# Optimization experiments

Measured on AMD Instinct MI355X. Metric: run time of the kernel, lower is better.

The kernel has to match this reference:

```python
import jax, jax.numpy as jnp
import numpy as np
import math

WINDOW = 2048
EMBED = 1024
BATCH = 8


def setup_inputs() -> dict:
    key = jax.random.key(0)
    ks = jax.random.split(key, 7)
    s = 1.0 / math.sqrt(EMBED)
    return {
        "embeddings": jax.random.normal(ks[0], (BATCH, WINDOW, EMBED), dtype=jnp.float32),
        "Wq": jax.random.uniform(ks[1], (EMBED, EMBED), jnp.float32, -s, s),
        "bq": jax.random.uniform(ks[2], (EMBED,), jnp.float32, -s, s),
        "Wk": jax.random.uniform(ks[3], (EMBED, EMBED), jnp.float32, -s, s),
        "bk": jax.random.uniform(ks[4], (EMBED,), jnp.float32, -s, s),
        "Wv": jax.random.uniform(ks[5], (EMBED, EMBED), jnp.float32, -s, s),
        "bv": jax.random.uniform(ks[6], (EMBED,), jnp.float32, -s, s),
    }


def reference(embeddings, Wq, bq, Wk, bk, Wv, bv):
    # Linear layers: x @ W.T + b (torch nn.Linear convention)
    Q = jnp.einsum('bse,fe->bsf', embeddings, Wq) + bq
    K = jnp.einsum('bse,fe->bsf', embeddings, Wk) + bk
    V = jnp.einsum('bse,fe->bsf', embeddings, Wv) + bv
    scale = 1.0 / math.sqrt(EMBED)
    # [B, S, S] score matrix: A[b, i, j] = Q_i . K_j / sqrt(d)
    A = jnp.einsum('bie,bje->bij', Q, K) * scale
    # causal additive mask: -inf where j > i (strictly upper triangular)
    mask = jnp.triu(jnp.full((WINDOW, WINDOW), -jnp.inf, dtype=A.dtype), k=1)
    A = A + mask
    # NOTE: faithful to original nn.Softmax(dim=1): normalize over QUERY axis
    P = jax.nn.softmax(A, axis=1)
    return jnp.einsum('bij,bje->bie', P, V)
```

## Files before the change

### kernel.cpp

```cpp
#include <hip/hip_runtime.h>
#include <stdint.h>

#define WINDOW 2048
#define EMBED  1024
#define BATCH  8
#define MTOT   (BATCH*WINDOW)

typedef unsigned short u16;
typedef __bf16 bf16x8 __attribute__((ext_vector_type(8)));
typedef float  f32x4  __attribute__((ext_vector_type(4)));

#define BK 64
#define KSCALE 0.04508422717564447f

#define BM2 256
#define BN2 256
#define HALF2 8192
#define PLD  260

#define WAITVM4 asm volatile("s_waitcnt vmcnt(4)" ::: "memory")
#define WAITVM0 asm volatile("s_waitcnt vmcnt(0)" ::: "memory")
#define SBAR    __builtin_amdgcn_s_barrier()

__device__ __forceinline__ u16 f2bf(float f) {
  union { float f; unsigned u; } a; a.f = f;
  unsigned r = a.u + 0x7FFF + ((a.u >> 16) & 1);
  return (u16)(r >> 16);
}
__device__ __forceinline__ float bf2f(u16 u) {
  union { unsigned u; float f; } a; a.u = ((unsigned)u) << 16;
  return a.f;
}

__device__ __forceinline__ void gload16(const u16* g, u16* l) {
  __builtin_amdgcn_global_load_lds(
      (const __attribute__((address_space(1))) unsigned int*)g,
      (__attribute__((address_space(3))) unsigned int*)l, 16, 0, 0);
}


__device__ __forceinline__ void gemm256(
    const u16* __restrict__ A, int lda,
    const u16* __restrict__ B, int ldb,
    int nt, u16* lds, f32x4 acc[8][4])
{
  const int tid  = threadIdx.x;
  const int lane = tid & 63;
  const int wid  = tid >> 6;
  const int wm   = (wid >> 2) * 128;
  const int wn   = (wid & 3) * 64;
  const int lrow = lane & 15;
  const int hi   = lane >> 4;
  u16* dA = lds;
  u16* dB = lds + 4 * HALF2;

  int aoff[8], boff[4];
  #pragma unroll
  for (int mi = 0; mi < 8; ++mi) {
    int r = wm + mi * 16 + lrow;
    aoff[mi] = r * 32 + ((hi ^ ((r >> 1) & 3)) << 3);
  }
  #pragma unroll
  for (int ni = 0; ni < 4; ++ni) {
    int r = wn + ni * 16 + lrow;
    boff[ni] = r * 32 + ((hi ^ ((r >> 1) & 3)) << 3);
  }

  const int f0 = tid, f1 = 512 + tid;
  const int r0 = f0 >> 2, r1 = f1 >> 2;
  const int c0 = (((f0 & 3) ^ ((r0 >> 1) & 3)) << 3);
  const int c1 = (((f1 & 3) ^ ((r1 >> 1) & 3)) << 3);
  const u16* pA0 = A + (size_t)r0 * lda + c0;
  const u16* pA1 = A + (size_t)r1 * lda + c1;
  const u16* pB0 = B + (size_t)r0 * ldb + c0;
  const u16* pB1 = B + (size_t)r1 * ldb + c1;
  const int d0 = f0 * 8, d1 = f1 * 8;

  gload16(pA0,      dA + d0);         gload16(pA1,      dA + d1);
  gload16(pB0,      dB + d0);         gload16(pB1,      dB + d1);
  gload16(pA0 + 32, dA + HALF2 + d0); gload16(pA1 + 32, dA + HALF2 + d1);
  gload16(pB0 + 32, dB + HALF2 + d0); gload16(pB1 + 32, dB + HALF2 + d1);
  pA0 += BK; pA1 += BK; pB0 += BK; pB1 += BK;
  WAITVM4;
  SBAR;

  for (int t = 0; t < nt; ++t) {
    const int cb = (t & 1) * 2;
    const int nb = ((t + 1) & 1) * 2;
    u16* LA0 = dA + cb * HALF2;  u16* LA1 = LA0 + HALF2;
    u16* LB0 = dB + cb * HALF2;  u16* LB1 = LB0 + HALF2;
    const bool s = (t + 1) < nt;
    bf16x8 av[8], bv[4];

    #pragma unroll
    for (int mi = 0; mi < 8; ++mi) av[mi] = *(const bf16x8*)(LA0 + aoff[mi]);
    #pragma unroll
    for (int ni = 0; ni < 4; ++ni) bv[ni] = *(const bf16x8*)(LB0 + boff[ni]);
    if (s) {
      gload16(pA0, dA + nb * HALF2 + d0); gload16(pA1, dA + nb * HALF2 + d1);
      gload16(pB0, dB + nb * HALF2 + d0); gload16(pB1, dB + nb * HALF2 + d1);
    }
    __builtin_amdgcn_s_setprio(1);
    #pragma unroll
    for (int mi = 0; mi < 8; ++mi)
      #pragma unroll
      for (int ni = 0; ni < 4; ++ni)
        acc[mi][ni] = __builtin_amdgcn_mfma_f32_16x16x32_bf16(av[mi], bv[ni], acc[mi][ni], 0, 0, 0);
    __builtin_amdgcn_s_setprio(0);
    if (s) { WAITVM4; } else { WAITVM0; }
    SBAR;

    #pragma unroll
    for (int mi = 0; mi < 8; ++mi) av[mi] = *(const bf16x8*)(LA1 + aoff[mi]);
    #pragma unroll
    for (int ni = 0; ni < 4; ++ni) bv[ni] = *(const bf16x8*)(LB1 + boff[ni]);
    if (s) {
      gload16(pA0 + 32, dA + nb * HALF2 + HALF2 + d0); gload16(pA1 + 32, dA + nb * HALF2 + HALF2 + d1);
      gload16(pB0 + 32, dB + nb * HALF2 + HALF2 + d0); gload16(pB1 + 32, dB + nb * HALF2 + HALF2 + d1);
      pA0 += BK; pA1 += BK; pB0 += BK; pB1 += BK;
    }
    __builtin_amdgcn_s_setprio(1);
    #pragma unroll
    for (int mi = 0; mi < 8; ++mi)
      #pragma unroll
      for (int ni = 0; ni < 4; ++ni)
        acc[mi][ni] = __builtin_amdgcn_mfma_f32_16x16x32_bf16(av[mi], bv[ni], acc[mi][ni], 0, 0, 0);
    __builtin_amdgcn_s_setprio(0);
    if (s) { WAITVM4; }
    SBAR;
  }
}

__global__ __launch_bounds__(256) void k_cvt(const float* __restrict__ in,
                                             u16* __restrict__ out, int n) {
  int i = (blockIdx.x * 256 + threadIdx.x) * 4;
  if (i >= n) return;
  float4 v = *(const float4*)(in + i);
  ushort4 o;
  o.x = f2bf(v.x); o.y = f2bf(v.y); o.z = f2bf(v.z); o.w = f2bf(v.w);
  *(ushort4*)(out + i) = o;
}

__global__ __launch_bounds__(256) void k_cvtw(const float* __restrict__ w0,
                                              const float* __restrict__ w1,
                                              const float* __restrict__ w2,
                                              u16* __restrict__ out) {
  const float* in = (blockIdx.y == 0) ? w0 : (blockIdx.y == 1) ? w1 : w2;
  u16* o = out + (size_t)blockIdx.y * EMBED * EMBED;
  int i = (blockIdx.x * 256 + threadIdx.x) * 4;
  float4 v = *(const float4*)(in + i);
  ushort4 r;
  r.x = f2bf(v.x); r.y = f2bf(v.y); r.z = f2bf(v.z); r.w = f2bf(v.w);
  *(ushort4*)(o + i) = r;
}

__global__ __launch_bounds__(512, 2) void k_qkv(
    const u16* __restrict__ Xb, const u16* __restrict__ Wb,
    const float* __restrict__ bq, const float* __restrict__ bk, const float* __restrict__ bv,
    u16* __restrict__ Q, u16* __restrict__ Ks, u16* __restrict__ V)
{
  __shared__ u16 lds[8 * HALF2];
  const int m0 = blockIdx.x * BM2;
  const int n0 = blockIdx.y * BN2;
  const int z  = blockIdx.z;
  const u16*   W    = Wb + (size_t)z * EMBED * EMBED;
  const float* bias = (z == 0) ? bq : (z == 1) ? bk : bv;
  u16* out          = (z == 0) ? Q  : (z == 1) ? Ks : V;
  const float scale = (z == 1) ? KSCALE : 1.0f;

  f32x4 acc[8][4];
  const f32x4 zz = {0.f,0.f,0.f,0.f};
  #pragma unroll
  for (int i = 0; i < 8; ++i) for (int j = 0; j < 4; ++j) acc[i][j] = zz;
  gemm256(Xb + (size_t)m0 * EMBED, EMBED, W + (size_t)n0 * EMBED, EMBED,
          EMBED / BK, lds, acc);

  const int lane = threadIdx.x & 63, wid = threadIdx.x >> 6;
  const int wm = (wid >> 2) * 128, wn = (wid & 3) * 64;
  const int lrow = lane & 15, hi = lane >> 4;
  #pragma unroll
  for (int mi = 0; mi < 8; ++mi)
    #pragma unroll
    for (int ni = 0; ni < 4; ++ni)
      #pragma unroll
      for (int rr = 0; rr < 4; ++rr) {
        int gm = m0 + wm + mi * 16 + hi * 4 + rr;
        int gn = n0 + wn + ni * 16 + lrow;
        out[(size_t)gm * EMBED + gn] = f2bf((acc[mi][ni][rr] + bias[gn]) * scale);
      }
}

__global__ __launch_bounds__(512, 2) void k_spd(
    const u16* __restrict__ Q, const u16* __restrict__ Ks,
    u16* __restrict__ P, float* __restrict__ D)
{
  const int s   = blockIdx.x;
  const int xcd = s & 7;
  const int q   = s >> 3;
  int it = 0;
  while (q >= ((it + 1) * (it + 2)) / 2) ++it;
  const int jt = q - (it * (it + 1)) / 2;
  const int b  = (xcd - it) & 7;
  const int i0 = it * BM2;
  const int j0 = jt * BN2;

  __shared__ u16 lds[BM2 * PLD];
  const u16* A = Q  + (size_t)b * WINDOW * EMBED + (size_t)i0 * EMBED;
  const u16* B = Ks + (size_t)b * WINDOW * EMBED + (size_t)j0 * EMBED;
  f32x4 acc[8][4];
  const f32x4 zz = {0.f,0.f,0.f,0.f};
  #pragma unroll
  for (int i = 0; i < 8; ++i) for (int j = 0; j < 4; ++j) acc[i][j] = zz;
  gemm256(A, EMBED, B, EMBED, EMBED / BK, lds, acc);

  u16* Pb   = P + (size_t)b * WINDOW * WINDOW;
  float* Db = D + (size_t)b * WINDOW;
  const int tid  = threadIdx.x;
  const int lane = tid & 63, wid = tid >> 6;
  const int wm = (wid >> 2) * 128, wn = (wid & 3) * 64;
  const int lrow = lane & 15, hi = lane >> 4;

  #pragma unroll
  for (int ni = 0; ni < 4; ++ni) {
    int lj = wn + ni * 16 + lrow;
    float csum = 0.f;
    #pragma unroll
    for (int mi = 0; mi < 8; ++mi)
      #pragma unroll
      for (int rr = 0; rr < 4; ++rr) {
        int li = wm + mi * 16 + hi * 4 + rr;
        float p = ((i0 + li) >= (j0 + lj)) ? exp2f(acc[mi][ni][rr]) : 0.0f;
        lds[li * PLD + lj] = f2bf(p);
        csum += p;
      }
    csum += __shfl_xor(csum, 16, 64);
    csum += __shfl_xor(csum, 32, 64);
    if (hi == 0) atomicAdd(&Db[j0 + lj], csum);
  }
  __syncthreads();

  #pragma unroll
  for (int it2 = 0; it2 < 16; ++it2) {
    int f   = it2 * 512 + tid;
    int row = f >> 5;
    int c   = f & 31;
    bf16x8 v = *(const bf16x8*)(lds + row * PLD + c * 8);
    *(bf16x8*)(Pb + (size_t)(i0 + row) * WINDOW + j0 + c * 8) = v;
  }
}

__global__ __launch_bounds__(256) void k_vdt(
    const u16* __restrict__ V, const float* __restrict__ D, u16* __restrict__ Vdt)
{
  __shared__ u16 tile[64][68];
  const int j0 = blockIdx.x * 64, e0 = blockIdx.y * 64, b = blockIdx.z;
  const u16* Vb = V   + (size_t)b * WINDOW * EMBED;
  u16* Tb       = Vdt + (size_t)b * EMBED * WINDOW;
  const float* Db = D + (size_t)b * WINDOW;
  const int t = threadIdx.x;
  const int rr = t >> 4;
  const int cc = (t & 15) * 4;
  #pragma unroll
  for (int p = 0; p < 4; ++p) {
    int r = p * 16 + rr;
    *(uint2*)&tile[r][cc] = *(const uint2*)(Vb + (size_t)(j0 + r) * EMBED + e0 + cc);
  }
  __syncthreads();
  #pragma unroll
  for (int p = 0; p < 4; ++p) {
    int er = p * 16 + rr;
    ushort4 o;
    o.x = f2bf(bf2f(tile[cc + 0][er]) / Db[j0 + cc + 0]);
    o.y = f2bf(bf2f(tile[cc + 1][er]) / Db[j0 + cc + 1]);
    o.z = f2bf(bf2f(tile[cc + 2][er]) / Db[j0 + cc + 2]);
    o.w = f2bf(bf2f(tile[cc + 3][er]) / Db[j0 + cc + 3]);
    *(ushort4*)(Tb + (size_t)(e0 + er) * WINDOW + j0 + cc) = o;
  }
}

__global__ __launch_bounds__(512, 2) void k_out(
    const u16* __restrict__ P, const u16* __restrict__ Vdt, float* __restrict__ O)
{
  __shared__ u16 lds[8 * HALF2];
  const int s   = blockIdx.x;
  const int xcd = s & 7;
  const int q   = s >> 3;
  const int et  = q & 3;
  const int it  = 7 - (q >> 2);
  const int b   = (xcd - it) & 7;
  const int i0  = it * BM2;
  const int e0  = et * BN2;

  const u16* A = P   + (size_t)b * WINDOW * WINDOW + (size_t)i0 * WINDOW;
  const u16* B = Vdt + (size_t)b * EMBED * WINDOW  + (size_t)e0 * WINDOW;
  f32x4 acc[8][4];
  const f32x4 zz = {0.f,0.f,0.f,0.f};
  #pragma unroll
  for (int i = 0; i < 8; ++i) for (int j = 0; j < 4; ++j) acc[i][j] = zz;
  gemm256(A, WINDOW, B, WINDOW, (i0 + BM2) / BK, lds, acc);

  float* Ob = O + (size_t)b * WINDOW * EMBED;
  const int lane = threadIdx.x & 63, wid = threadIdx.x >> 6;
  const int wm = (wid >> 2) * 128, wn = (wid & 3) * 64;
  const int lrow = lane & 15, hi = lane >> 4;
  #pragma unroll
  for (int mi = 0; mi < 8; ++mi)
    #pragma unroll
    for (int ni = 0; ni < 4; ++ni)
      #pragma unroll
      for (int rr = 0; rr < 4; ++rr) {
        int gi = i0 + wm + mi * 16 + hi * 4 + rr;
        int ge = e0 + wn + ni * 16 + lrow;
        Ob[(size_t)gi * EMBED + ge] = acc[mi][ni][rr];
      }
}

extern "C" void kernel_launch(void* const* d_in, const int* in_sizes, int n_in,
                              void* d_out, int out_size, void* d_ws, size_t ws_size,
                              hipStream_t stream) {
  const float* X  = (const float*)d_in[0];
  const float* Wq = (const float*)d_in[1];
  const float* bq = (const float*)d_in[2];
  const float* Wk = (const float*)d_in[3];
  const float* bk = (const float*)d_in[4];
  const float* Wv = (const float*)d_in[5];
  const float* bv = (const float*)d_in[6];
  float* O = (float*)d_out;

  char* ws = (char*)d_ws;
  size_t off = 0;
  auto alloc = [&](size_t bytes) -> void* {
    void* p = ws + off; off += (bytes + 255) & ~(size_t)255; return p;
  };
  u16*  Xb  = (u16*)alloc((size_t)MTOT * EMBED * 2);
  u16*  Wb  = (u16*)alloc((size_t)3 * EMBED * EMBED * 2);
  u16*  Qb  = (u16*)alloc((size_t)MTOT * EMBED * 2);
  u16*  Kb  = (u16*)alloc((size_t)MTOT * EMBED * 2);
  u16*  Vb  = (u16*)alloc((size_t)MTOT * EMBED * 2);
  u16*  Vdt = (u16*)alloc((size_t)BATCH * EMBED * WINDOW * 2);
  u16*  P   = (u16*)alloc((size_t)BATCH * WINDOW * WINDOW * 2);
  float* D  = (float*)alloc((size_t)MTOT * 4);
  (void)ws_size; (void)in_sizes; (void)n_in; (void)out_size;

  k_cvt<<<dim3((MTOT * EMBED / 4 + 255) / 256), 256, 0, stream>>>(X, Xb, MTOT * EMBED);
  k_cvtw<<<dim3(EMBED * EMBED / 4 / 256, 3), 256, 0, stream>>>(Wq, Wk, Wv, Wb);

  k_qkv<<<dim3(MTOT / BM2, EMBED / BN2, 3), 512, 0, stream>>>(Xb, Wb, bq, bk, bv, Qb, Kb, Vb);

  (void)hipMemsetAsync(D, 0, (size_t)MTOT * 4, stream);
  k_spd<<<dim3(288), 512, 0, stream>>>(Qb, Kb, P, D);

  k_vdt<<<dim3(WINDOW / 64, EMBED / 64, BATCH), 256, 0, stream>>>(Vb, D, Vdt);

  k_out<<<dim3(256), 512, 0, stream>>>(P, Vdt, O);
}
```

Baseline: 281.9 us.

## Fold Q/K projections into X·(Wqᵀ·Wk) with row-bias term exploiting query-axis softmax

Because the softmax normalizes over the query axis, score terms that depend only on the key index cancel. The scores can therefore be rewritten as x_i·H·x_jᵀ + u_i, with H = scale·Wqᵀ·Wk and u_i = x_i·(Wqᵀ·bk). The change precomputes H with a split-K 128-tile GEMM plus a reduction, computes u alongside the X conversion, and replaces the three-way QKV projection with two GEMMs (X·H and X·Wv). The score kernel then multiplies Y by X directly. This removes one large projection GEMM and its output writes. In exchange it adds several small kernels, including a latency-bound k_w loop, and adds bf16 rounding of H.

```diff
diff --git a/kernel.cpp b/kernel.cpp
--- a/kernel.cpp
+++ b/kernel.cpp
@@ -17,8 +17,10 @@
 #define BN2 256
 #define HALF2 8192
 #define PLD  260
+#define HALF1 4096
 
 #define WAITVM4 asm volatile("s_waitcnt vmcnt(4)" ::: "memory")
+#define WAITVM2 asm volatile("s_waitcnt vmcnt(2)" ::: "memory")
 #define WAITVM0 asm volatile("s_waitcnt vmcnt(0)" ::: "memory")
 #define SBAR    __builtin_amdgcn_s_barrier()
 
@@ -131,6 +133,145 @@
   }
 }
 
+__device__ __forceinline__ void gemm128(
+    const u16* __restrict__ A, int lda,
+    const u16* __restrict__ B, int ldb,
+    int nt, u16* lds, f32x4 acc[4][2])
+{
+  const int tid  = threadIdx.x;
+  const int lane = tid & 63;
+  const int wid  = tid >> 6;
+  const int wm   = (wid >> 2) * 64;
+  const int wn   = (wid & 3) * 32;
+  const int lrow = lane & 15;
+  const int hi   = lane >> 4;
+  u16* dA = lds;
+  u16* dB = lds + 4 * HALF1;
+
+  const int r = tid >> 2;
+  const int cs = (((tid & 3) ^ ((r >> 1) & 3)) << 3);
+  const u16* pA = A + (size_t)r * lda + cs;
+  const u16* pB = B + (size_t)r * ldb + cs;
+  const int d = tid * 8;
+
+  gload16(pA,      dA + d);         gload16(pB,      dB + d);
+  gload16(pA + 32, dA + HALF1 + d); gload16(pB + 32, dB + HALF1 + d);
+  pA += BK; pB += BK;
+  WAITVM2;
+  SBAR;
+
+  for (int t = 0; t < nt; ++t) {
+    const int cur = (t & 1) * 2;
+    const int nxt = ((t + 1) & 1) * 2;
+    u16* LA0 = dA + cur * HALF1;  u16* LA1 = LA0 + HALF1;
+    u16* LB0 = dB + cur * HALF1;  u16* LB1 = LB0 + HALF1;
+    const bool s = (t + 1) < nt;
+    bf16x8 av[4], bv[2];
+
+    #pragma unroll
+    for (int mi = 0; mi < 4; ++mi) {
+      int rr = wm + mi * 16 + lrow;
+      av[mi] = *(const bf16x8*)(LA0 + rr * 32 + ((hi ^ ((rr >> 1) & 3)) << 3));
+    }
+    #pragma unroll
+    for (int ni = 0; ni < 2; ++ni) {
+      int rr = wn + ni * 16 + lrow;
+      bv[ni] = *(const bf16x8*)(LB0 + rr * 32 + ((hi ^ ((rr >> 1) & 3)) << 3));
+    }
+    if (s) { gload16(pA, dA + nxt * HALF1 + d); gload16(pB, dB + nxt * HALF1 + d); }
+    #pragma unroll
+    for (int mi = 0; mi < 4; ++mi)
+      #pragma unroll
+      for (int ni = 0; ni < 2; ++ni)
+        acc[mi][ni] = __builtin_amdgcn_mfma_f32_16x16x32_bf16(av[mi], bv[ni], acc[mi][ni], 0, 0, 0);
+    if (s) { WAITVM2; } else { WAITVM0; }
+    SBAR;
+
+    #pragma unroll
+    for (int mi = 0; mi < 4; ++mi) {
+      int rr = wm + mi * 16 + lrow;
+      av[mi] = *(const bf16x8*)(LA1 + rr * 32 + ((hi ^ ((rr >> 1) & 3)) << 3));
+    }
+    #pragma unroll
+    for (int ni = 0; ni < 2; ++ni) {
+      int rr = wn + ni * 16 + lrow;
+      bv[ni] = *(const bf16x8*)(LB1 + rr * 32 + ((hi ^ ((rr >> 1) & 3)) << 3));
+    }
+    if (s) {
+      gload16(pA + 32, dA + nxt * HALF1 + HALF1 + d);
+      gload16(pB + 32, dB + nxt * HALF1 + HALF1 + d);
+      pA += BK; pB += BK;
+    }
+    #pragma unroll
+    for (int mi = 0; mi < 4; ++mi)
+      #pragma unroll
+      for (int ni = 0; ni < 2; ++ni)
+        acc[mi][ni] = __builtin_amdgcn_mfma_f32_16x16x32_bf16(av[mi], bv[ni], acc[mi][ni], 0, 0, 0);
+    if (s) { WAITVM2; }
+    SBAR;
+  }
+}
+
+__global__ __launch_bounds__(256) void k_w(const float* __restrict__ Wq,
+                                           const float* __restrict__ bk,
+                                           float* __restrict__ w) {
+  const int e = blockIdx.x * 256 + threadIdx.x;
+  float acc = 0.f;
+  #pragma unroll 4
+  for (int f = 0; f < EMBED; ++f)
+    acc += Wq[(size_t)f * EMBED + e] * bk[f];
+  w[e] = acc * KSCALE;
+}
+
+__global__ __launch_bounds__(256) void k_cvtu(const float* __restrict__ X,
+                                              const float* __restrict__ w,
+                                              u16* __restrict__ Xb,
+                                              float* __restrict__ u) {
+  const int row = blockIdx.x;
+  const int tid = threadIdx.x;
+  float4 v  = *(const float4*)(X + (size_t)row * EMBED + tid * 4);
+  float4 ww = *(const float4*)(w + tid * 4);
+  ushort4 o;
+  o.x = f2bf(v.x); o.y = f2bf(v.y); o.z = f2bf(v.z); o.w = f2bf(v.w);
+  *(ushort4*)(Xb + (size_t)row * EMBED + tid * 4) = o;
+  float p = v.x * ww.x + v.y * ww.y + v.z * ww.z + v.w * ww.w;
+  #pragma unroll
+  for (int off = 1; off < 64; off <<= 1) p += __shfl_xor(p, off, 64);
+  __shared__ float red[4];
+  if ((tid & 63) == 0) red[tid >> 6] = p;
+  __syncthreads();
+  if (tid == 0) u[row] = red[0] + red[1] + red[2] + red[3];
+}
+
+__global__ __launch_bounds__(256) void k_trw(const float* __restrict__ Wq,
+                                             const float* __restrict__ Wk,
+                                             u16* __restrict__ WqT,
+                                             u16* __restrict__ WkT) {
+  __shared__ u16 tile[64][68];
+  const float* in = blockIdx.z ? Wk : Wq;
+  u16* out        = blockIdx.z ? WkT : WqT;
+  const int f0 = blockIdx.x * 64, e0 = blockIdx.y * 64;
+  const int t = threadIdx.x;
+  const int rr = t >> 4;
+  const int cc = (t & 15) * 4;
+  #pragma unroll
+  for (int p = 0; p < 4; ++p) {
+    int r = p * 16 + rr;
+    float4 v = *(const float4*)(in + (size_t)(f0 + r) * EMBED + e0 + cc);
+    tile[r][cc + 0] = f2bf(v.x); tile[r][cc + 1] = f2bf(v.y);
+    tile[r][cc + 2] = f2bf(v.z); tile[r][cc + 3] = f2bf(v.w);
+  }
+  __syncthreads();
+  #pragma unroll
+  for (int p = 0; p < 4; ++p) {
+    int er = p * 16 + rr;
+    ushort4 o;
+    o.x = tile[cc + 0][er]; o.y = tile[cc + 1][er];
+    o.z = tile[cc + 2][er]; o.w = tile[cc + 3][er];
+    *(ushort4*)(out + (size_t)(e0 + er) * EMBED + f0 + cc) = o;
+  }
+}
+
 __global__ __launch_bounds__(256) void k_cvt(const float* __restrict__ in,
                                              u16* __restrict__ out, int n) {
   int i = (blockIdx.x * 256 + threadIdx.x) * 4;
@@ -141,38 +282,70 @@
   *(ushort4*)(out + i) = o;
 }
 
-__global__ __launch_bounds__(256) void k_cvtw(const float* __restrict__ w0,
-                                              const float* __restrict__ w1,
-                                              const float* __restrict__ w2,
-                                              u16* __restrict__ out) {
-  const float* in = (blockIdx.y == 0) ? w0 : (blockIdx.y == 1) ? w1 : w2;
-  u16* o = out + (size_t)blockIdx.y * EMBED * EMBED;
+__global__ __launch_bounds__(512, 4) void k_H(const u16* __restrict__ WkT,
+                                              const u16* __restrict__ WqT,
+                                              float* __restrict__ Hws) {
+  __shared__ u16 lds[8 * HALF1];
+  const int s  = blockIdx.x & 3;
+  const int tt = blockIdx.x >> 2;
+  const int a0 = (tt >> 3) * 128, b0 = (tt & 7) * 128;
+  const u16* A = WkT + (size_t)a0 * EMBED + s * 256;
+  const u16* B = WqT + (size_t)b0 * EMBED + s * 256;
+  f32x4 acc[4][2];
+  const f32x4 zz = {0.f,0.f,0.f,0.f};
+  #pragma unroll
+  for (int i = 0; i < 4; ++i) for (int j = 0; j < 2; ++j) acc[i][j] = zz;
+  gemm128(A, EMBED, B, EMBED, 4, lds, acc);
+
+  float* Hp = Hws + (size_t)s * EMBED * EMBED;
+  const int lane = threadIdx.x & 63, wid = threadIdx.x >> 6;
+  const int wm = (wid >> 2) * 64, wn = (wid & 3) * 32;
+  const int lrow = lane & 15, hi = lane >> 4;
+  #pragma unroll
+  for (int mi = 0; mi < 4; ++mi)
+    #pragma unroll
+    for (int ni = 0; ni < 2; ++ni)
+      #pragma unroll
+      for (int rr = 0; rr < 4; ++rr) {
+        int ga = a0 + wm + mi * 16 + hi * 4 + rr;
+        int gb = b0 + wn + ni * 16 + lrow;
+        Hp[(size_t)ga * EMBED + gb] = acc[mi][ni][rr];
+      }
+}
+
+__global__ __launch_bounds__(256) void k_Hred(const float* __restrict__ Hws,
+                                              u16* __restrict__ H) {
+  const size_t N = (size_t)EMBED * EMBED;
   int i = (blockIdx.x * 256 + threadIdx.x) * 4;
-  float4 v = *(const float4*)(in + i);
-  ushort4 r;
-  r.x = f2bf(v.x); r.y = f2bf(v.y); r.z = f2bf(v.z); r.w = f2bf(v.w);
-  *(ushort4*)(o + i) = r;
-}
-
-__global__ __launch_bounds__(512, 2) void k_qkv(
-    const u16* __restrict__ Xb, const u16* __restrict__ Wb,
-    const float* __restrict__ bq, const float* __restrict__ bk, const float* __restrict__ bv,
-    u16* __restrict__ Q, u16* __restrict__ Ks, u16* __restrict__ V)
+  float4 a = *(const float4*)(Hws + i);
+  float4 b = *(const float4*)(Hws + N + i);
+  float4 c = *(const float4*)(Hws + 2 * N + i);
+  float4 d = *(const float4*)(Hws + 3 * N + i);
+  ushort4 o;
+  o.x = f2bf((a.x + b.x + c.x + d.x) * KSCALE);
+  o.y = f2bf((a.y + b.y + c.y + d.y) * KSCALE);
+  o.z = f2bf((a.z + b.z + c.z + d.z) * KSCALE);
+  o.w = f2bf((a.w + b.w + c.w + d.w) * KSCALE);
+  *(ushort4*)(H + i) = o;
+}
+
+__global__ __launch_bounds__(512, 2) void k_yv(
+    const u16* __restrict__ Xb, const u16* __restrict__ H,
+    const u16* __restrict__ Wvb, const float* __restrict__ bv,
+    u16* __restrict__ Yb, u16* __restrict__ Vb)
 {
   __shared__ u16 lds[8 * HALF2];
   const int m0 = blockIdx.x * BM2;
   const int n0 = blockIdx.y * BN2;
   const int z  = blockIdx.z;
-  const u16*   W    = Wb + (size_t)z * EMBED * EMBED;
-  const float* bias = (z == 0) ? bq : (z == 1) ? bk : bv;
-  u16* out          = (z == 0) ? Q  : (z == 1) ? Ks : V;
-  const float scale = (z == 1) ? KSCALE : 1.0f;
+  const u16* Bop = z ? Wvb : H;
+  u16* out       = z ? Vb : Yb;
 
   f32x4 acc[8][4];
   const f32x4 zz = {0.f,0.f,0.f,0.f};
   #pragma unroll
   for (int i = 0; i < 8; ++i) for (int j = 0; j < 4; ++j) acc[i][j] = zz;
-  gemm256(Xb + (size_t)m0 * EMBED, EMBED, W + (size_t)n0 * EMBED, EMBED,
+  gemm256(Xb + (size_t)m0 * EMBED, EMBED, Bop + (size_t)n0 * EMBED, EMBED,
           EMBED / BK, lds, acc);
 
   const int lane = threadIdx.x & 63, wid = threadIdx.x >> 6;
@@ -186,13 +359,14 @@
       for (int rr = 0; rr < 4; ++rr) {
         int gm = m0 + wm + mi * 16 + hi * 4 + rr;
         int gn = n0 + wn + ni * 16 + lrow;
-        out[(size_t)gm * EMBED + gn] = f2bf((acc[mi][ni][rr] + bias[gn]) * scale);
+        float bb = z ? bv[gn] : 0.0f;
+        out[(size_t)gm * EMBED + gn] = f2bf(acc[mi][ni][rr] + bb);
       }
 }
 
 __global__ __launch_bounds__(512, 2) void k_spd(
-    const u16* __restrict__ Q, const u16* __restrict__ Ks,
-    u16* __restrict__ P, float* __restrict__ D)
+    const u16* __restrict__ Y, const u16* __restrict__ Xb,
+    const float* __restrict__ u, u16* __restrict__ P, float* __restrict__ D)
 {
   const int s   = blockIdx.x;
   const int xcd = s & 7;
@@ -205,8 +379,8 @@
   const int j0 = jt * BN2;
 
   __shared__ u16 lds[BM2 * PLD];
-  const u16* A = Q  + (size_t)b * WINDOW * EMBED + (size_t)i0 * EMBED;
-  const u16* B = Ks + (size_t)b * WINDOW * EMBED + (size_t)j0 * EMBED;
+  const u16* A = Y  + (size_t)b * WINDOW * EMBED + (size_t)i0 * EMBED;
+  const u16* B = Xb + (size_t)b * WINDOW * EMBED + (size_t)j0 * EMBED;
   f32x4 acc[8][4];
   const f32x4 zz = {0.f,0.f,0.f,0.f};
   #pragma unroll
@@ -215,6 +389,7 @@
 
   u16* Pb   = P + (size_t)b * WINDOW * WINDOW;
   float* Db = D + (size_t)b * WINDOW;
+  const float* ub = u + (size_t)b * WINDOW;
   const int tid  = threadIdx.x;
   const int lane = tid & 63, wid = tid >> 6;
   const int wm = (wid >> 2) * 128, wn = (wid & 3) * 64;
@@ -229,7 +404,8 @@
       #pragma unroll
       for (int rr = 0; rr < 4; ++rr) {
         int li = wm + mi * 16 + hi * 4 + rr;
-        float p = ((i0 + li) >= (j0 + lj)) ? exp2f(acc[mi][ni][rr]) : 0.0f;
+        float p = ((i0 + li) >= (j0 + lj))
+                    ? exp2f(acc[mi][ni][rr] + ub[i0 + li]) : 0.0f;
         lds[li * PLD + lj] = f2bf(p);
         csum += p;
       }
@@ -326,29 +502,39 @@
   const float* Wv = (const float*)d_in[5];
   const float* bv = (const float*)d_in[6];
   float* O = (float*)d_out;
+  (void)bq;
 
   char* ws = (char*)d_ws;
   size_t off = 0;
   auto alloc = [&](size_t bytes) -> void* {
     void* p = ws + off; off += (bytes + 255) & ~(size_t)255; return p;
   };
-  u16*  Xb  = (u16*)alloc((size_t)MTOT * EMBED * 2);
-  u16*  Wb  = (u16*)alloc((size_t)3 * EMBED * EMBED * 2);
-  u16*  Qb  = (u16*)alloc((size_t)MTOT * EMBED * 2);
-  u16*  Kb  = (u16*)alloc((size_t)MTOT * EMBED * 2);
-  u16*  Vb  = (u16*)alloc((size_t)MTOT * EMBED * 2);
-  u16*  Vdt = (u16*)alloc((size_t)BATCH * EMBED * WINDOW * 2);
-  u16*  P   = (u16*)alloc((size_t)BATCH * WINDOW * WINDOW * 2);
-  float* D  = (float*)alloc((size_t)MTOT * 4);
+  u16*   Xb  = (u16*)alloc((size_t)MTOT * EMBED * 2);
+  u16*   Yb  = (u16*)alloc((size_t)MTOT * EMBED * 2);
+  u16*   Vb  = (u16*)alloc((size_t)MTOT * EMBED * 2);
+  u16*   Vdt = (u16*)alloc((size_t)BATCH * EMBED * WINDOW * 2);
+  u16*   P   = (u16*)alloc((size_t)BATCH * WINDOW * WINDOW * 2);
+  u16*   WqT = (u16*)alloc((size_t)EMBED * EMBED * 2);
+  u16*   WkT = (u16*)alloc((size_t)EMBED * EMBED * 2);
+  u16*   Wvb = (u16*)alloc((size_t)EMBED * EMBED * 2);
+  u16*   H   = (u16*)alloc((size_t)EMBED * EMBED * 2);
+  float* Hws = (float*)alloc((size_t)4 * EMBED * EMBED * 4);
+  float* w   = (float*)alloc((size_t)EMBED * 4);
+  float* u   = (float*)alloc((size_t)MTOT * 4);
+  float* D   = (float*)alloc((size_t)MTOT * 4);
   (void)ws_size; (void)in_sizes; (void)n_in; (void)out_size;
 
-  k_cvt<<<dim3((MTOT * EMBED / 4 + 255) / 256), 256, 0, stream>>>(X, Xb, MTOT * EMBED);
-  k_cvtw<<<dim3(EMBED * EMBED / 4 / 256, 3), 256, 0, stream>>>(Wq, Wk, Wv, Wb);
-
-  k_qkv<<<dim3(MTOT / BM2, EMBED / BN2, 3), 512, 0, stream>>>(Xb, Wb, bq, bk, bv, Qb, Kb, Vb);
+  k_w<<<dim3(EMBED / 256), 256, 0, stream>>>(Wq, bk, w);
+  k_cvtu<<<dim3(MTOT), 256, 0, stream>>>(X, w, Xb, u);
+  k_trw<<<dim3(16, 16, 2), 256, 0, stream>>>(Wq, Wk, WqT, WkT);
+  k_cvt<<<dim3(EMBED * EMBED / 1024), 256, 0, stream>>>(Wv, Wvb, EMBED * EMBED);
+  k_H<<<dim3(256), 512, 0, stream>>>(WkT, WqT, Hws);
+  k_Hred<<<dim3(EMBED * EMBED / 1024), 256, 0, stream>>>(Hws, H);
+
+  k_yv<<<dim3(MTOT / BM2, EMBED / BN2, 2), 512, 0, stream>>>(Xb, H, Wvb, bv, Yb, Vb);
 
   (void)hipMemsetAsync(D, 0, (size_t)MTOT * 4, stream);
-  k_spd<<<dim3(288), 512, 0, stream>>>(Qb, Kb, P, D);
+  k_spd<<<dim3(288), 512, 0, stream>>>(Yb, Xb, u, P, D);
 
   k_vdt<<<dim3(WINDOW / 64, EMBED / 64, BATCH), 256, 0, stream>>>(Vb, D, Vdt);
 
```

After: 385.5 us. +36.7%, slower.
